# Kernel optimization log

Measured on AMD Instinct MI355X. Metric: run time of the kernel, lower is better.

Reference implementation:

```python
import jax, jax.numpy as jnp
import numpy as np

LN_EPS = 1e-3  # keras LayerNormalization default


def setup_inputs() -> dict:
    key = jax.random.key(0)
    k1, k2, k3 = jax.random.split(key, 3)
    B, T, D, H = 64, 512, 256, 512
    inputs = jax.random.normal(k1, (B, T, D), dtype=jnp.float32)
    h0 = jnp.zeros((B, H), dtype=jnp.float32)
    Wx = jax.random.normal(k2, (D, H), dtype=jnp.float32) / np.sqrt(D)
    Wh = jax.random.normal(k3, (H, H), dtype=jnp.float32) / np.sqrt(H)
    b = jnp.zeros((H,), dtype=jnp.float32)
    gamma = jnp.ones((H,), dtype=jnp.float32)
    beta = jnp.zeros((H,), dtype=jnp.float32)
    return {"inputs": inputs, "h0": h0, "Wx": Wx, "Wh": Wh, "b": b,
            "gamma": gamma, "beta": beta}


def _layer_norm(x, gamma, beta):
    mu = jnp.mean(x, axis=-1, keepdims=True)
    var = jnp.mean(jnp.square(x - mu), axis=-1, keepdims=True)
    return (x - mu) * jax.lax.rsqrt(var + LN_EPS) * gamma + beta


def reference(inputs, h0, Wx, Wh, b, gamma, beta):
    # Precompute input projection for all timesteps: [B, T, H]
    xproj = jnp.einsum('btd,dh->bth', inputs, Wx) + b

    def step(h, xp_t):
        z = xp_t + h @ Wh                      # SimpleRNNCell, activation=None
        h_new = jnp.tanh(_layer_norm(z, gamma, beta))
        return h_new, h_new

    _, outs = jax.lax.scan(step, h0, jnp.swapaxes(xproj, 0, 1))
    return jnp.swapaxes(outs, 0, 1)            # [B, T, H]
```

## Files before the change

### kernel.cpp

```cpp
#include <hip/hip_runtime.h>
#include <cstdint>
#include <cstddef>

#define T_STEPS 512
#define D_DIM 256
#define H_DIM 512
#define B_SZ 64

#define NCG 8
#define CGW (H_DIM / NCG)
#define NTH 512


#define BM 64
#define BN 128
#define BK 32

__global__ __launch_bounds__(256)
void xproj_gemm(const float* __restrict__ A, const float* __restrict__ Bm,
                const float* __restrict__ bias, float* __restrict__ C,
                int M, int N, int K) {
    __shared__ float As[BK][BM];
    __shared__ float Bs[BK][BN];

    const int tid = threadIdx.x;
    const int tx = tid & 15;
    const int ty = tid >> 4;
    const int row0 = blockIdx.y * BM;
    const int col0 = blockIdx.x * BN;

    float acc[4][8];
    #pragma unroll
    for (int i = 0; i < 4; ++i)
        #pragma unroll
        for (int j = 0; j < 8; ++j) acc[i][j] = 0.0f;

    for (int kt = 0; kt < K; kt += BK) {
        #pragma unroll
        for (int i = 0; i < 2; ++i) {
            int q  = tid + i * 256;
            int m  = q >> 3;
            int k4 = (q & 7) << 2;
            float4 v = *(const float4*)&A[(size_t)(row0 + m) * K + kt + k4];
            As[k4 + 0][m] = v.x; As[k4 + 1][m] = v.y;
            As[k4 + 2][m] = v.z; As[k4 + 3][m] = v.w;
        }
        #pragma unroll
        for (int i = 0; i < 4; ++i) {
            int q  = tid + i * 256;
            int kk = q >> 5;
            int n4 = (q & 31) << 2;
            *(float4*)&Bs[kk][n4] = *(const float4*)&Bm[(size_t)(kt + kk) * N + col0 + n4];
        }
        __syncthreads();
        #pragma unroll
        for (int k = 0; k < BK; ++k) {
            float4 a  = *(const float4*)&As[k][ty << 2];
            float4 b0 = *(const float4*)&Bs[k][tx << 2];
            float4 b1 = *(const float4*)&Bs[k][(tx << 2) + 64];
            float av[4] = {a.x, a.y, a.z, a.w};
            float bv[8] = {b0.x, b0.y, b0.z, b0.w, b1.x, b1.y, b1.z, b1.w};
            #pragma unroll
            for (int i = 0; i < 4; ++i)
                #pragma unroll
                for (int j = 0; j < 8; ++j)
                    acc[i][j] = fmaf(av[i], bv[j], acc[i][j]);
        }
        __syncthreads();
    }

    float bv0[4], bv1[4];
    #pragma unroll
    for (int j = 0; j < 4; ++j) {
        bv0[j] = bias[col0 + (tx << 2) + j];
        bv1[j] = bias[col0 + (tx << 2) + 64 + j];
    }
    #pragma unroll
    for (int i = 0; i < 4; ++i) {
        int r = row0 + (ty << 2) + i;
        float4 o0 = make_float4(acc[i][0] + bv0[0], acc[i][1] + bv0[1],
                                acc[i][2] + bv0[2], acc[i][3] + bv0[3]);
        float4 o1 = make_float4(acc[i][4] + bv1[0], acc[i][5] + bv1[1],
                                acc[i][6] + bv1[2], acc[i][7] + bv1[3]);
        *(float4*)&C[(size_t)r * N + col0 + (tx << 2)]      = o0;
        *(float4*)&C[(size_t)r * N + col0 + (tx << 2) + 64] = o1;
    }
}

__device__ __forceinline__ float tanh_fast(float x) {
    float ax = fabsf(x);
    float e  = __expf(2.0f * ax);
    float t  = 1.0f - 2.0f / (e + 1.0f);
    return copysignf(t, x);
}

__global__ __launch_bounds__(NTH, 4)
void rnn_scan6(const float* __restrict__ Wh, const float* __restrict__ h0,
               const float* __restrict__ gamma, const float* __restrict__ beta,
               float* __restrict__ out,
               unsigned long long* __restrict__ zbuf) {
    const int cg  = blockIdx.x & (NCG - 1);
    const int r   = blockIdx.x >> 3;
    const int tid = threadIdx.x;
    const int c   = tid & (CGW - 1);
    const int kc  = tid >> 6;

    __shared__ float h_s[H_DIM];
    __shared__ float part_s[NCG][CGW];
    __shared__ float wred_s[16];

    float w[64];
    #pragma unroll
    for (int j = 0; j < 64; ++j)
        w[j] = Wh[(size_t)(kc * CGW + j) * H_DIM + cg * CGW + c];

    h_s[tid] = h0[r * H_DIM + tid];
    const float g_own = gamma[tid];
    const float b_own = beta[tid];
    float* outrow = out + (size_t)r * T_STEPS * H_DIM;
    unsigned long long* zrow0 = zbuf + (size_t)(r * 2) * H_DIM;

    float xp_next = 0.0f;
    if (tid < CGW)
        xp_next = __builtin_nontemporal_load(&outrow[cg * CGW + tid]);
    __syncthreads();

    for (int t = 0; t < T_STEPS; ++t) {
        unsigned long long* zrow = zrow0 + (size_t)(t & 1) * H_DIM;
        const unsigned int tag = (unsigned int)(t + 1);
        const float xp = xp_next;

        const float4* h4 = (const float4*)&h_s[kc * CGW];
        float a0 = 0.0f, a1 = 0.0f, a2 = 0.0f, a3 = 0.0f;
        #pragma unroll
        for (int j4 = 0; j4 < 16; ++j4) {
            float4 hv = h4[j4];
            a0 = fmaf(w[4 * j4 + 0], hv.x, a0);
            a1 = fmaf(w[4 * j4 + 1], hv.y, a1);
            a2 = fmaf(w[4 * j4 + 2], hv.z, a2);
            a3 = fmaf(w[4 * j4 + 3], hv.w, a3);
        }
        part_s[kc][c] = (a0 + a1) + (a2 + a3);
        __syncthreads();

        if (tid < CGW) {
            float z = xp;
            #pragma unroll
            for (int k = 0; k < NCG; ++k) z += part_s[k][tid];
            unsigned long long pkt = ((unsigned long long)tag << 32)
                                   | (unsigned long long)__float_as_uint(z);
            __hip_atomic_store(&zrow[cg * CGW + tid], pkt,
                               __ATOMIC_RELAXED, __HIP_MEMORY_SCOPE_AGENT);
        }

        if (tid < CGW && t + 1 < T_STEPS)
            xp_next = __builtin_nontemporal_load(
                &outrow[(size_t)(t + 1) * H_DIM + cg * CGW + tid]);

        unsigned long long pkt;
        do {
            pkt = __hip_atomic_load(&zrow[tid], __ATOMIC_RELAXED,
                                    __HIP_MEMORY_SCOPE_AGENT);
        } while ((unsigned int)(pkt >> 32) != tag);
        float z = __uint_as_float((unsigned int)pkt);

        float s = z, q = z * z;
        #pragma unroll
        for (int o = 32; o > 0; o >>= 1) {
            s += __shfl_down(s, o, 64);
            q += __shfl_down(q, o, 64);
        }
        if ((tid & 63) == 0) { wred_s[kc] = s; wred_s[8 + kc] = q; }
        __syncthreads();
        float S = 0.0f, Q = 0.0f;
        #pragma unroll
        for (int i = 0; i < 8; ++i) { S += wred_s[i]; Q += wred_s[8 + i]; }
        float mean = S * (1.0f / H_DIM);
        float var  = Q * (1.0f / H_DIM) - mean * mean;
        float rstd = rsqrtf(var + 1e-3f);

        float hn = tanh_fast((z - mean) * rstd * g_own + b_own);
        if (kc == cg)
            __builtin_nontemporal_store(hn, &outrow[(size_t)t * H_DIM + tid]);
        h_s[tid] = hn;
        __syncthreads();
    }
}

extern "C" void kernel_launch(void* const* d_in, const int* in_sizes, int n_in,
                              void* d_out, int out_size, void* d_ws, size_t ws_size,
                              hipStream_t stream) {
    const float* inputs = (const float*)d_in[0];
    const float* h0     = (const float*)d_in[1];
    const float* Wx     = (const float*)d_in[2];
    const float* Wh     = (const float*)d_in[3];
    const float* bias   = (const float*)d_in[4];
    const float* gamma  = (const float*)d_in[5];
    const float* beta   = (const float*)d_in[6];
    float* out = (float*)d_out;

    unsigned long long* zbuf = (unsigned long long*)d_ws;

    const int M = B_SZ * T_STEPS;
    dim3 g1(H_DIM / BN, M / BM);
    xproj_gemm<<<g1, 256, 0, stream>>>(inputs, Wx, bias, out, M, H_DIM, D_DIM);

    rnn_scan6<<<B_SZ * NCG, NTH, 0, stream>>>(Wh, h0, gamma, beta, out, zbuf);
}
```

Baseline: 1.265 ms.

## Fuse input projection into recurrent scan kernel and skip own-slice polling

Removes the separate input-projection GEMM kernel and computes each step's x_t·Wx inside the scan. Each block keeps its slice of Wx in registers and double-buffers the input row in shared memory. Blocks also take their own column group's z values directly instead of polling them back through global memory. This adds 32 more weight registers per thread and extra FMAs on the serial critical path of every step, in exchange for removing a kernel launch and the xproj round trip through the output buffer.

```diff
diff --git a/kernel.cpp b/kernel.cpp
--- a/kernel.cpp
+++ b/kernel.cpp
@@ -12,81 +12,6 @@
 #define NTH 512
 
 
-#define BM 64
-#define BN 128
-#define BK 32
-
-__global__ __launch_bounds__(256)
-void xproj_gemm(const float* __restrict__ A, const float* __restrict__ Bm,
-                const float* __restrict__ bias, float* __restrict__ C,
-                int M, int N, int K) {
-    __shared__ float As[BK][BM];
-    __shared__ float Bs[BK][BN];
-
-    const int tid = threadIdx.x;
-    const int tx = tid & 15;
-    const int ty = tid >> 4;
-    const int row0 = blockIdx.y * BM;
-    const int col0 = blockIdx.x * BN;
-
-    float acc[4][8];
-    #pragma unroll
-    for (int i = 0; i < 4; ++i)
-        #pragma unroll
-        for (int j = 0; j < 8; ++j) acc[i][j] = 0.0f;
-
-    for (int kt = 0; kt < K; kt += BK) {
-        #pragma unroll
-        for (int i = 0; i < 2; ++i) {
-            int q  = tid + i * 256;
-            int m  = q >> 3;
-            int k4 = (q & 7) << 2;
-            float4 v = *(const float4*)&A[(size_t)(row0 + m) * K + kt + k4];
-            As[k4 + 0][m] = v.x; As[k4 + 1][m] = v.y;
-            As[k4 + 2][m] = v.z; As[k4 + 3][m] = v.w;
-        }
-        #pragma unroll
-        for (int i = 0; i < 4; ++i) {
-            int q  = tid + i * 256;
-            int kk = q >> 5;
-            int n4 = (q & 31) << 2;
-            *(float4*)&Bs[kk][n4] = *(const float4*)&Bm[(size_t)(kt + kk) * N + col0 + n4];
-        }
-        __syncthreads();
-        #pragma unroll
-        for (int k = 0; k < BK; ++k) {
-            float4 a  = *(const float4*)&As[k][ty << 2];
-            float4 b0 = *(const float4*)&Bs[k][tx << 2];
-            float4 b1 = *(const float4*)&Bs[k][(tx << 2) + 64];
-            float av[4] = {a.x, a.y, a.z, a.w};
-            float bv[8] = {b0.x, b0.y, b0.z, b0.w, b1.x, b1.y, b1.z, b1.w};
-            #pragma unroll
-            for (int i = 0; i < 4; ++i)
-                #pragma unroll
-                for (int j = 0; j < 8; ++j)
-                    acc[i][j] = fmaf(av[i], bv[j], acc[i][j]);
-        }
-        __syncthreads();
-    }
-
-    float bv0[4], bv1[4];
-    #pragma unroll
-    for (int j = 0; j < 4; ++j) {
-        bv0[j] = bias[col0 + (tx << 2) + j];
-        bv1[j] = bias[col0 + (tx << 2) + 64 + j];
-    }
-    #pragma unroll
-    for (int i = 0; i < 4; ++i) {
-        int r = row0 + (ty << 2) + i;
-        float4 o0 = make_float4(acc[i][0] + bv0[0], acc[i][1] + bv0[1],
-                                acc[i][2] + bv0[2], acc[i][3] + bv0[3]);
-        float4 o1 = make_float4(acc[i][4] + bv1[0], acc[i][5] + bv1[1],
-                                acc[i][6] + bv1[2], acc[i][7] + bv1[3]);
-        *(float4*)&C[(size_t)r * N + col0 + (tx << 2)]      = o0;
-        *(float4*)&C[(size_t)r * N + col0 + (tx << 2) + 64] = o1;
-    }
-}
-
 __device__ __forceinline__ float tanh_fast(float x) {
     float ax = fabsf(x);
     float e  = __expf(2.0f * ax);
@@ -95,10 +20,12 @@
 }
 
 __global__ __launch_bounds__(NTH, 4)
-void rnn_scan6(const float* __restrict__ Wh, const float* __restrict__ h0,
-               const float* __restrict__ gamma, const float* __restrict__ beta,
-               float* __restrict__ out,
-               unsigned long long* __restrict__ zbuf) {
+void rnn_fused8(const float* __restrict__ Wh, const float* __restrict__ Wx,
+                const float* __restrict__ inputs, const float* __restrict__ h0,
+                const float* __restrict__ bias,
+                const float* __restrict__ gamma, const float* __restrict__ beta,
+                float* __restrict__ out,
+                unsigned long long* __restrict__ zbuf) {
     const int cg  = blockIdx.x & (NCG - 1);
     const int r   = blockIdx.x >> 3;
     const int tid = threadIdx.x;
@@ -106,63 +33,85 @@
     const int kc  = tid >> 6;
 
     __shared__ float h_s[H_DIM];
+    __shared__ float x_s[2][D_DIM];
     __shared__ float part_s[NCG][CGW];
     __shared__ float wred_s[16];
 
     float w[64];
     #pragma unroll
     for (int j = 0; j < 64; ++j)
-        w[j] = Wh[(size_t)(kc * CGW + j) * H_DIM + cg * CGW + c];
+        w[j] = Wh[(size_t)(kc * 64 + j) * H_DIM + cg * CGW + c];
+
+    float wx[32];
+    #pragma unroll
+    for (int j = 0; j < 32; ++j)
+        wx[j] = Wx[(size_t)(kc * 32 + j) * H_DIM + cg * CGW + c];
 
     h_s[tid] = h0[r * H_DIM + tid];
+    const float* inrow = inputs + (size_t)r * T_STEPS * D_DIM;
+    if (tid < D_DIM) x_s[0][tid] = inrow[tid];
+
     const float g_own = gamma[tid];
     const float b_own = beta[tid];
+    const float b_pub = bias[cg * CGW + c];
     float* outrow = out + (size_t)r * T_STEPS * H_DIM;
     unsigned long long* zrow0 = zbuf + (size_t)(r * 2) * H_DIM;
-
-    float xp_next = 0.0f;
-    if (tid < CGW)
-        xp_next = __builtin_nontemporal_load(&outrow[cg * CGW + tid]);
     __syncthreads();
 
     for (int t = 0; t < T_STEPS; ++t) {
         unsigned long long* zrow = zrow0 + (size_t)(t & 1) * H_DIM;
         const unsigned int tag = (unsigned int)(t + 1);
-        const float xp = xp_next;
 
-        const float4* h4 = (const float4*)&h_s[kc * CGW];
         float a0 = 0.0f, a1 = 0.0f, a2 = 0.0f, a3 = 0.0f;
-        #pragma unroll
-        for (int j4 = 0; j4 < 16; ++j4) {
-            float4 hv = h4[j4];
-            a0 = fmaf(w[4 * j4 + 0], hv.x, a0);
-            a1 = fmaf(w[4 * j4 + 1], hv.y, a1);
-            a2 = fmaf(w[4 * j4 + 2], hv.z, a2);
-            a3 = fmaf(w[4 * j4 + 3], hv.w, a3);
+        {
+            const float4* h4 = (const float4*)&h_s[kc * CGW];
+            #pragma unroll
+            for (int j4 = 0; j4 < 16; ++j4) {
+                float4 hv = h4[j4];
+                a0 = fmaf(w[4 * j4 + 0], hv.x, a0);
+                a1 = fmaf(w[4 * j4 + 1], hv.y, a1);
+                a2 = fmaf(w[4 * j4 + 2], hv.z, a2);
+                a3 = fmaf(w[4 * j4 + 3], hv.w, a3);
+            }
+            const float4* x4 = (const float4*)&x_s[t & 1][kc * 32];
+            #pragma unroll
+            for (int j4 = 0; j4 < 8; ++j4) {
+                float4 xv = x4[j4];
+                a0 = fmaf(wx[4 * j4 + 0], xv.x, a0);
+                a1 = fmaf(wx[4 * j4 + 1], xv.y, a1);
+                a2 = fmaf(wx[4 * j4 + 2], xv.z, a2);
+                a3 = fmaf(wx[4 * j4 + 3], xv.w, a3);
+            }
         }
         part_s[kc][c] = (a0 + a1) + (a2 + a3);
         __syncthreads();
 
+        float zloc = b_pub;
+        #pragma unroll
+        for (int k = 0; k < NCG; ++k) zloc += part_s[k][c];
+
         if (tid < CGW) {
-            float z = xp;
-            #pragma unroll
-            for (int k = 0; k < NCG; ++k) z += part_s[k][tid];
             unsigned long long pkt = ((unsigned long long)tag << 32)
-                                   | (unsigned long long)__float_as_uint(z);
+                                   | (unsigned long long)__float_as_uint(zloc);
             __hip_atomic_store(&zrow[cg * CGW + tid], pkt,
                                __ATOMIC_RELAXED, __HIP_MEMORY_SCOPE_AGENT);
         }
 
-        if (tid < CGW && t + 1 < T_STEPS)
-            xp_next = __builtin_nontemporal_load(
-                &outrow[(size_t)(t + 1) * H_DIM + cg * CGW + tid]);
+        const int tn = (t + 1 < T_STEPS) ? t + 1 : t;
+        float xnext = 0.0f;
+        if (tid < D_DIM) xnext = inrow[(size_t)tn * D_DIM + tid];
 
-        unsigned long long pkt;
-        do {
-            pkt = __hip_atomic_load(&zrow[tid], __ATOMIC_RELAXED,
-                                    __HIP_MEMORY_SCOPE_AGENT);
-        } while ((unsigned int)(pkt >> 32) != tag);
-        float z = __uint_as_float((unsigned int)pkt);
+        float z;
+        if (kc == cg) {
+            z = zloc;
+        } else {
+            unsigned long long pkt;
+            do {
+                pkt = __hip_atomic_load(&zrow[tid], __ATOMIC_RELAXED,
+                                        __HIP_MEMORY_SCOPE_AGENT);
+            } while ((unsigned int)(pkt >> 32) != tag);
+            z = __uint_as_float((unsigned int)pkt);
+        }
 
         float s = z, q = z * z;
         #pragma unroll
@@ -180,9 +129,9 @@
         float rstd = rsqrtf(var + 1e-3f);
 
         float hn = tanh_fast((z - mean) * rstd * g_own + b_own);
-        if (kc == cg)
-            __builtin_nontemporal_store(hn, &outrow[(size_t)t * H_DIM + tid]);
+        if (kc == cg) outrow[(size_t)t * H_DIM + tid] = hn;
         h_s[tid] = hn;
+        if (tid < D_DIM) x_s[(t + 1) & 1][tid] = xnext;
         __syncthreads();
     }
 }
@@ -201,9 +150,6 @@
 
     unsigned long long* zbuf = (unsigned long long*)d_ws;
 
-    const int M = B_SZ * T_STEPS;
-    dim3 g1(H_DIM / BN, M / BM);
-    xproj_gemm<<<g1, 256, 0, stream>>>(inputs, Wx, bias, out, M, H_DIM, D_DIM);
-
-    rnn_scan6<<<B_SZ * NCG, NTH, 0, stream>>>(Wh, h0, gamma, beta, out, zbuf);
+    rnn_fused8<<<B_SZ * NCG, NTH, 0, stream>>>(Wh, Wx, inputs, h0, bias,
+                                               gamma, beta, out, zbuf);
 }
```

New measurement: 1.731 ms. 1.37x slower.
